# Optimization experiments

Measured on AMD Instinct MI355X. Metric: run time of the kernel, lower is better.

The kernel has to match this reference:

```python
import jax, jax.numpy as jnp
import numpy as np

EPS = 1e-6

def setup_inputs() -> dict:
    key = jax.random.key(0)
    ks = jax.random.split(key, 4)
    T, B, D, N = 512, 16, 1024, 512
    # xavier-uniform-ish scale for projections
    lim = float(np.sqrt(6.0 / (N + D)))
    x = jax.random.normal(ks[0], (T, B, D), dtype=jnp.float32)
    W_k = jax.random.uniform(ks[1], (N, D), minval=-lim, maxval=lim, dtype=jnp.float32)
    W_v = jax.random.uniform(ks[2], (N, D), minval=-lim, maxval=lim, dtype=jnp.float32)
    W_q = jax.random.uniform(ks[3], (N, D), minval=-lim, maxval=lim, dtype=jnp.float32)
    return {"x": x, "W_k": W_k, "W_v": W_v, "W_q": W_q}

def reference(x, W_k, W_v, W_q):
    # x: (T, B, D); delta-rule fast-weight cell, proj=no_z, nonlin=tanh,
    # gate=output, update=delta.
    T, B, D = x.shape
    n = W_k.shape[0]
    k = jnp.einsum('tbd,nd->tbn', x, W_k)
    v = jnp.einsum('tbd,nd->tbn', x, W_v)
    q = jnp.einsum('tbd,nd->tbn', x, W_q)
    k_norm = k / (jnp.linalg.norm(k, axis=-1, keepdims=True) + EPS)

    def step(S, kvq):
        k_t, v_t, q_t = kvq  # each (B, n)
        retrieved = jnp.einsum('bij,bj->bi', S, k_t)
        delta = v_t - retrieved
        S_new = jnp.tanh(S + delta[:, :, None] * k_t[:, None, :])
        Sq = jnp.einsum('bij,bj->bi', S_new, q_t)
        out = Sq * jax.nn.silu(Sq)
        return S_new, out

    S0 = jnp.zeros((B, n, n), dtype=x.dtype)
    S_final, outputs = jax.lax.scan(step, S0, (k_norm, v, q))
    return outputs, S_final
```

## Files before the change

kernel.cpp:

```cpp
#include <hip/hip_runtime.h>
#include <hip/hip_bf16.h>

#define T_DIM 512
#define B_DIM 16
#define D_DIM 1024
#define N_DIM 512

#define C_FOLD  2.885390082f
#define INV_C   0.3465735903f

typedef short s16x8 __attribute__((ext_vector_type(8)));
typedef float f32x4 __attribute__((ext_vector_type(4)));
typedef float f32x2 __attribute__((ext_vector_type(2)));

__device__ __forceinline__ unsigned short f2bf(float f) {
    unsigned u = __float_as_uint(f);
    unsigned r = (u + 0x7fffu + ((u >> 16) & 1u)) >> 16;
    return (unsigned short)r;
}

__device__ __forceinline__ float half32_sum(float x) {
    x += __int_as_float(__builtin_amdgcn_update_dpp(0, __float_as_int(x), 0xB1,  0xf, 0xf, true));
    x += __int_as_float(__builtin_amdgcn_update_dpp(0, __float_as_int(x), 0x4E,  0xf, 0xf, true));
    x += __int_as_float(__builtin_amdgcn_update_dpp(0, __float_as_int(x), 0x124, 0xf, 0xf, true));
    x += __int_as_float(__builtin_amdgcn_update_dpp(0, __float_as_int(x), 0x128, 0xf, 0xf, true));
    x += __int_as_float(__builtin_amdgcn_ds_swizzle(__float_as_int(x), 0x401F));
    return x;
}

__device__ __forceinline__ f32x2 tanh2p(f32x2 arg, f32x2 Cv, f32x2 M2Cv) {
    float e0 = __builtin_amdgcn_exp2f(arg.x) + 1.0f;
    float e1 = __builtin_amdgcn_exp2f(arg.y) + 1.0f;
    float r  = __builtin_amdgcn_rcpf(e0 * e1);
    f32x2 w; w.x = e1 * r; w.y = e0 * r;
    return Cv + w * M2Cv;
}

__global__ __launch_bounds__(256) void proj_gemm(
    const float* __restrict__ x,
    const float* __restrict__ Wk,
    const float* __restrict__ Wv,
    const float* __restrict__ Wq,
    float* __restrict__ kbuf, float* __restrict__ vbuf, float* __restrict__ qbuf)
{
    const float* W = (blockIdx.z == 0) ? Wk : (blockIdx.z == 1) ? Wv : Wq;
    float* out = (blockIdx.z == 0) ? kbuf : (blockIdx.z == 1) ? vbuf : qbuf;
    const float oscale = (blockIdx.z == 1) ? C_FOLD : 1.0f;

    __shared__ __align__(16) unsigned short As[64 * 40];
    __shared__ __align__(16) unsigned short Bs[64 * 40];

    const int tid  = threadIdx.x;
    const int m0   = blockIdx.x * 64;
    const int n0   = blockIdx.y * 64;
    const int wave = tid >> 6;
    const int lane = tid & 63;
    const int l15  = lane & 15;
    const int quad = lane >> 4;

    const int srow = tid >> 2;
    const int scol = (tid & 3) * 8;

    f32x4 acc[4];
#pragma unroll
    for (int i = 0; i < 4; ++i) acc[i] = (f32x4)0.0f;

    for (int k0 = 0; k0 < D_DIM; k0 += 32) {
        __syncthreads();
        {
            const float* srcA = &x[(size_t)(m0 + srow) * D_DIM + k0 + scol];
            float4 a0 = *(const float4*)srcA;
            float4 a1 = *(const float4*)(srcA + 4);
            uint4 pa;
            pa.x = (unsigned)f2bf(a0.x) | ((unsigned)f2bf(a0.y) << 16);
            pa.y = (unsigned)f2bf(a0.z) | ((unsigned)f2bf(a0.w) << 16);
            pa.z = (unsigned)f2bf(a1.x) | ((unsigned)f2bf(a1.y) << 16);
            pa.w = (unsigned)f2bf(a1.z) | ((unsigned)f2bf(a1.w) << 16);
            *(uint4*)&As[srow * 40 + scol] = pa;

            const float* srcB = &W[(size_t)(n0 + srow) * D_DIM + k0 + scol];
            float4 b0 = *(const float4*)srcB;
            float4 b1 = *(const float4*)(srcB + 4);
            uint4 pb;
            pb.x = (unsigned)f2bf(b0.x) | ((unsigned)f2bf(b0.y) << 16);
            pb.y = (unsigned)f2bf(b0.z) | ((unsigned)f2bf(b0.w) << 16);
            pb.z = (unsigned)f2bf(b1.x) | ((unsigned)f2bf(b1.y) << 16);
            pb.w = (unsigned)f2bf(b1.z) | ((unsigned)f2bf(b1.w) << 16);
            *(uint4*)&Bs[srow * 40 + scol] = pb;
        }
        __syncthreads();
        s16x8 af = *(const s16x8*)&As[(wave * 16 + l15) * 40 + quad * 8];
#pragma unroll
        for (int nt = 0; nt < 4; ++nt) {
            s16x8 bf = *(const s16x8*)&Bs[(nt * 16 + l15) * 40 + quad * 8];
            acc[nt] = __builtin_amdgcn_mfma_f32_16x16x32_bf16(af, bf, acc[nt], 0, 0, 0);
        }
    }
#pragma unroll
    for (int nt = 0; nt < 4; ++nt) {
#pragma unroll
        for (int rg = 0; rg < 4; ++rg) {
            int row = m0 + wave * 16 + quad * 4 + rg;
            int col = n0 + nt * 16 + l15;
            out[(size_t)row * N_DIM + col] = acc[nt][rg] * oscale;
        }
    }
}

__global__ __launch_bounds__(256) void knorm(float* __restrict__ kbuf)
{
    const int wave = threadIdx.x >> 6;
    const int lane = threadIdx.x & 63;
    const int row  = blockIdx.x * 4 + wave;
    float* p = &kbuf[(size_t)row * N_DIM + lane * 8];
    float4 a = *(const float4*)p;
    float4 b = *(const float4*)(p + 4);
    float s = a.x*a.x + a.y*a.y + a.z*a.z + a.w*a.w
            + b.x*b.x + b.y*b.y + b.z*b.z + b.w*b.w;
#pragma unroll
    for (int m = 1; m < 64; m <<= 1) s += __shfl_xor(s, m, 64);
    float inv = 1.0f / (sqrtf(s) + 1e-6f);
    a.x *= inv; a.y *= inv; a.z *= inv; a.w *= inv;
    b.x *= inv; b.y *= inv; b.z *= inv; b.w *= inv;
    *(float4*)p = a;
    *(float4*)(p + 4) = b;
}

__global__ __launch_bounds__(256) void scan_kernel(
    const float* __restrict__ kbuf, const float* __restrict__ vbuf,
    const float* __restrict__ qbuf, float* __restrict__ out)
{
    __shared__ __align__(16) float ks[2][528];
    __shared__ __align__(16) float qs[2][528];
    __shared__ float vs[2][16];

    const int tid  = threadIdx.x;
    const int lane = tid & 63;
    const int wv   = tid >> 6;
    const int h    = lane >> 5;
    const int tj   = lane & 31;
    const int b    = blockIdx.y;
    const int i0   = blockIdx.x * 16;
    const int r0   = 4 * wv + 2 * h;

    const int wA = 33 * (tid >> 4) + ((2 * tid) & 31);
    const int rA = 33 * (tj >> 1) + 16 * (tj & 1);

    f32x2 SA[8], SB[8];
#pragma unroll
    for (int u = 0; u < 8; ++u) { SA[u] = (f32x2)0.0f; SB[u] = (f32x2)0.0f; }

    float2 pk, pq; float pv = 0.0f;
    {
        const size_t o0 = (size_t)b * N_DIM;
        pk = *(const float2*)&kbuf[o0 + 2 * tid];
        pq = *(const float2*)&qbuf[o0 + 2 * tid];
        if (tid < 16) pv = vbuf[o0 + i0 + tid];
        *(float2*)&ks[0][wA] = pk;
        *(float2*)&qs[0][wA] = pq;
        if (tid < 16) vs[0][tid] = pv;
        const size_t o1 = (size_t)(B_DIM + b) * N_DIM;
        pk = *(const float2*)&kbuf[o1 + 2 * tid];
        pq = *(const float2*)&qbuf[o1 + 2 * tid];
        if (tid < 16) pv = vbuf[o1 + i0 + tid];
    }
    __syncthreads();

    const f32x2 Cv   = {C_FOLD, C_FOLD};
    const f32x2 M2Cv = {-2.0f * C_FOLD, -2.0f * C_FOLD};

    for (int t = 0; t < T_DIM; ++t) {
        const int cb = t & 1, nb = cb ^ 1;
        const size_t ofs = ((size_t)t * B_DIM + b) * N_DIM;

        if (t + 1 < T_DIM) {
            *(float2*)&ks[nb][wA] = pk;
            *(float2*)&qs[nb][wA] = pq;
            if (tid < 16) vs[nb][tid] = pv;
        }
        if (t + 2 < T_DIM) {
            const size_t o2 = ((size_t)(t + 2) * B_DIM + b) * N_DIM;
            pk = *(const float2*)&kbuf[o2 + 2 * tid];
            pq = *(const float2*)&qbuf[o2 + 2 * tid];
            if (tid < 16) pv = vbuf[o2 + i0 + tid];
        }

        f32x2 k2[8], q2[8];
#pragma unroll
        for (int u = 0; u < 4; ++u) {
            f32x4 kv = *(const f32x4*)&ks[cb][rA + 4 * u];
            f32x4 qv = *(const f32x4*)&qs[cb][rA + 4 * u];
            k2[2*u] = kv.xy; k2[2*u+1] = kv.zw;
            q2[2*u] = qv.xy; q2[2*u+1] = qv.zw;
        }
        const float v0 = vs[cb][r0];
        const float v1 = vs[cb][r0 + 1];

        f32x2 pa0 = (f32x2)0.0f, pb0 = (f32x2)0.0f;
        f32x2 pa1 = (f32x2)0.0f, pb1 = (f32x2)0.0f;
#pragma unroll
        for (int u = 0; u < 8; u += 2) {
            pa0 += SA[u] * k2[u];  pb0 += SA[u + 1] * k2[u + 1];
            pa1 += SB[u] * k2[u];  pb1 += SB[u + 1] * k2[u + 1];
        }
        const float racc0 = half32_sum(pa0.x + pa0.y + pb0.x + pb0.y);
        const float racc1 = half32_sum(pa1.x + pa1.y + pb1.x + pb1.y);

        const float dp0 = v0 - racc0;
        const float dp1 = v1 - racc1;
        const f32x2 d0 = {dp0, dp0}, d1 = {dp1, dp1};

        f32x2 sa0 = (f32x2)0.0f, sb0 = (f32x2)0.0f;
        f32x2 sa1 = (f32x2)0.0f, sb1 = (f32x2)0.0f;
#pragma unroll
        for (int u = 0; u < 8; u += 2) {
            f32x2 nA0 = tanh2p(SA[u]     + d0 * k2[u],     Cv, M2Cv);
            f32x2 nB0 = tanh2p(SB[u]     + d1 * k2[u],     Cv, M2Cv);
            f32x2 nA1 = tanh2p(SA[u + 1] + d0 * k2[u + 1], Cv, M2Cv);
            f32x2 nB1 = tanh2p(SB[u + 1] + d1 * k2[u + 1], Cv, M2Cv);
            SA[u] = nA0; SB[u] = nB0; SA[u + 1] = nA1; SB[u + 1] = nB1;
            sa0 += nA0 * q2[u];     sa1 += nB0 * q2[u];
            sb0 += nA1 * q2[u + 1]; sb1 += nB1 * q2[u + 1];
        }
        const float sq0 = half32_sum(sa0.x + sa0.y + sb0.x + sb0.y);
        const float sq1 = half32_sum(sa1.x + sa1.y + sb1.x + sb1.y);

        if (tj == 0) {
            float s0 = sq0 * INV_C, s1 = sq1 * INV_C;
            float g0 = __builtin_amdgcn_rcpf(1.0f + __builtin_amdgcn_exp2f(-s0 * 1.44269504f));
            float g1 = __builtin_amdgcn_rcpf(1.0f + __builtin_amdgcn_exp2f(-s1 * 1.44269504f));
            out[ofs + i0 + r0]     = s0 * s0 * g0;
            out[ofs + i0 + r0 + 1] = s1 * s1 * g1;
        }
        __syncthreads();
    }

    const size_t base = (size_t)T_DIM * B_DIM * N_DIM;
    const size_t so0 = base + ((size_t)b * N_DIM + i0 + r0) * N_DIM + 16 * tj;
    const size_t so1 = so0 + N_DIM;
#pragma unroll
    for (int u = 0; u < 4; ++u) {
        float4 w0, w1;
        w0.x = SA[2*u].x   * INV_C; w0.y = SA[2*u].y   * INV_C;
        w0.z = SA[2*u+1].x * INV_C; w0.w = SA[2*u+1].y * INV_C;
        w1.x = SB[2*u].x   * INV_C; w1.y = SB[2*u].y   * INV_C;
        w1.z = SB[2*u+1].x * INV_C; w1.w = SB[2*u+1].y * INV_C;
        *(float4*)&out[so0 + 4 * u] = w0;
        *(float4*)&out[so1 + 4 * u] = w1;
    }
}

extern "C" void kernel_launch(void* const* d_in, const int* in_sizes, int n_in,
                              void* d_out, int out_size, void* d_ws, size_t ws_size,
                              hipStream_t stream) {
    const float* x  = (const float*)d_in[0];
    const float* Wk = (const float*)d_in[1];
    const float* Wv = (const float*)d_in[2];
    const float* Wq = (const float*)d_in[3];
    float* outp = (float*)d_out;

    const size_t MN = (size_t)T_DIM * B_DIM * N_DIM;
    float* kbuf = (float*)d_ws;
    float* vbuf = kbuf + MN;
    float* qbuf = vbuf + MN;

    proj_gemm<<<dim3(128, 8, 3), 256, 0, stream>>>(x, Wk, Wv, Wq, kbuf, vbuf, qbuf);
    knorm<<<2048, 256, 0, stream>>>(kbuf);
    scan_kernel<<<dim3(32, 16), 256, 0, stream>>>(kbuf, vbuf, qbuf, outp);
}
```

Before: 797.1 us.

## Load k/q/v directly into registers per step, drop LDS staging and barriers

The scan loop no longer stages k, q and v through double-buffered shared memory with a block-wide barrier every timestep. Each lane now reads its own 16 k and 16 q values and its two v values straight from global memory into registers, one step ahead, with the loop unrolled by two to ping-pong between register sets. This removes the per-step __syncthreads and the LDS writes and reads. In exchange every lane issues redundant global loads (32 lanes share the same k/q slice, and each 16-row block rereads them), and the prefetch distance shrinks from two steps to one, so more global latency may be exposed.

```diff
diff --git a/kernel.cpp b/kernel.cpp
--- a/kernel.cpp
+++ b/kernel.cpp
@@ -130,10 +130,6 @@
     const float* __restrict__ kbuf, const float* __restrict__ vbuf,
     const float* __restrict__ qbuf, float* __restrict__ out)
 {
-    __shared__ __align__(16) float ks[2][528];
-    __shared__ __align__(16) float qs[2][528];
-    __shared__ float vs[2][16];
-
     const int tid  = threadIdx.x;
     const int lane = tid & 63;
     const int wv   = tid >> 6;
@@ -143,97 +139,90 @@
     const int i0   = blockIdx.x * 16;
     const int r0   = 4 * wv + 2 * h;
 
-    const int wA = 33 * (tid >> 4) + ((2 * tid) & 31);
-    const int rA = 33 * (tj >> 1) + 16 * (tj & 1);
+    const size_t BSTR = (size_t)B_DIM * N_DIM;
+    const float* kbase = kbuf + (size_t)b * N_DIM + 16 * tj;
+    const float* qbase = qbuf + (size_t)b * N_DIM + 16 * tj;
+    const float* vbase = vbuf + (size_t)b * N_DIM + i0 + r0;
 
     f32x2 SA[8], SB[8];
 #pragma unroll
     for (int u = 0; u < 8; ++u) { SA[u] = (f32x2)0.0f; SB[u] = (f32x2)0.0f; }
-
-    float2 pk, pq; float pv = 0.0f;
-    {
-        const size_t o0 = (size_t)b * N_DIM;
-        pk = *(const float2*)&kbuf[o0 + 2 * tid];
-        pq = *(const float2*)&qbuf[o0 + 2 * tid];
-        if (tid < 16) pv = vbuf[o0 + i0 + tid];
-        *(float2*)&ks[0][wA] = pk;
-        *(float2*)&qs[0][wA] = pq;
-        if (tid < 16) vs[0][tid] = pv;
-        const size_t o1 = (size_t)(B_DIM + b) * N_DIM;
-        pk = *(const float2*)&kbuf[o1 + 2 * tid];
-        pq = *(const float2*)&qbuf[o1 + 2 * tid];
-        if (tid < 16) pv = vbuf[o1 + i0 + tid];
-    }
-    __syncthreads();
 
     const f32x2 Cv   = {C_FOLD, C_FOLD};
     const f32x2 M2Cv = {-2.0f * C_FOLD, -2.0f * C_FOLD};
 
-    for (int t = 0; t < T_DIM; ++t) {
-        const int cb = t & 1, nb = cb ^ 1;
-        const size_t ofs = ((size_t)t * B_DIM + b) * N_DIM;
-
-        if (t + 1 < T_DIM) {
-            *(float2*)&ks[nb][wA] = pk;
-            *(float2*)&qs[nb][wA] = pq;
-            if (tid < 16) vs[nb][tid] = pv;
-        }
-        if (t + 2 < T_DIM) {
-            const size_t o2 = ((size_t)(t + 2) * B_DIM + b) * N_DIM;
-            pk = *(const float2*)&kbuf[o2 + 2 * tid];
-            pq = *(const float2*)&qbuf[o2 + 2 * tid];
-            if (tid < 16) pv = vbuf[o2 + i0 + tid];
-        }
-
-        f32x2 k2[8], q2[8];
-#pragma unroll
-        for (int u = 0; u < 4; ++u) {
-            f32x4 kv = *(const f32x4*)&ks[cb][rA + 4 * u];
-            f32x4 qv = *(const f32x4*)&qs[cb][rA + 4 * u];
-            k2[2*u] = kv.xy; k2[2*u+1] = kv.zw;
-            q2[2*u] = qv.xy; q2[2*u+1] = qv.zw;
-        }
-        const float v0 = vs[cb][r0];
-        const float v1 = vs[cb][r0 + 1];
-
-        f32x2 pa0 = (f32x2)0.0f, pb0 = (f32x2)0.0f;
-        f32x2 pa1 = (f32x2)0.0f, pb1 = (f32x2)0.0f;
-#pragma unroll
-        for (int u = 0; u < 8; u += 2) {
-            pa0 += SA[u] * k2[u];  pb0 += SA[u + 1] * k2[u + 1];
-            pa1 += SB[u] * k2[u];  pb1 += SB[u + 1] * k2[u + 1];
-        }
-        const float racc0 = half32_sum(pa0.x + pa0.y + pb0.x + pb0.y);
-        const float racc1 = half32_sum(pa1.x + pa1.y + pb1.x + pb1.y);
-
-        const float dp0 = v0 - racc0;
-        const float dp1 = v1 - racc1;
-        const f32x2 d0 = {dp0, dp0}, d1 = {dp1, dp1};
-
-        f32x2 sa0 = (f32x2)0.0f, sb0 = (f32x2)0.0f;
-        f32x2 sa1 = (f32x2)0.0f, sb1 = (f32x2)0.0f;
-#pragma unroll
-        for (int u = 0; u < 8; u += 2) {
-            f32x2 nA0 = tanh2p(SA[u]     + d0 * k2[u],     Cv, M2Cv);
-            f32x2 nB0 = tanh2p(SB[u]     + d1 * k2[u],     Cv, M2Cv);
-            f32x2 nA1 = tanh2p(SA[u + 1] + d0 * k2[u + 1], Cv, M2Cv);
-            f32x2 nB1 = tanh2p(SB[u + 1] + d1 * k2[u + 1], Cv, M2Cv);
-            SA[u] = nA0; SB[u] = nB0; SA[u + 1] = nA1; SB[u + 1] = nB1;
-            sa0 += nA0 * q2[u];     sa1 += nB0 * q2[u];
-            sb0 += nA1 * q2[u + 1]; sb1 += nB1 * q2[u + 1];
-        }
-        const float sq0 = half32_sum(sa0.x + sa0.y + sb0.x + sb0.y);
-        const float sq1 = half32_sum(sa1.x + sa1.y + sb1.x + sb1.y);
-
-        if (tj == 0) {
-            float s0 = sq0 * INV_C, s1 = sq1 * INV_C;
-            float g0 = __builtin_amdgcn_rcpf(1.0f + __builtin_amdgcn_exp2f(-s0 * 1.44269504f));
-            float g1 = __builtin_amdgcn_rcpf(1.0f + __builtin_amdgcn_exp2f(-s1 * 1.44269504f));
-            out[ofs + i0 + r0]     = s0 * s0 * g0;
-            out[ofs + i0 + r0 + 1] = s1 * s1 * g1;
-        }
-        __syncthreads();
-    }
+    f32x4 kA[4], qA[4], kB[4], qB[4];
+    float2 vA, vB;
+
+#pragma unroll
+    for (int u = 0; u < 4; ++u) {
+        kA[u] = *(const f32x4*)(kbase + 4 * u);
+        qA[u] = *(const f32x4*)(qbase + 4 * u);
+    }
+    vA = *(const float2*)vbase;
+
+#define SCAN_STEP(T_IDX, KC, QC, VC, KN, QN, VN)                              \
+    {                                                                         \
+        const int tn = ((T_IDX) + 1 < T_DIM) ? (T_IDX) + 1 : (T_DIM - 1);     \
+        const float* kpn = kbase + (size_t)tn * BSTR;                         \
+        const float* qpn = qbase + (size_t)tn * BSTR;                         \
+        _Pragma("unroll")                                                     \
+        for (int u = 0; u < 4; ++u) {                                         \
+            KN[u] = *(const f32x4*)(kpn + 4 * u);                             \
+            QN[u] = *(const f32x4*)(qpn + 4 * u);                             \
+        }                                                                     \
+        VN = *(const float2*)(vbase + (size_t)tn * BSTR);                     \
+                                                                              \
+        f32x2 k2[8], q2[8];                                                   \
+        _Pragma("unroll")                                                     \
+        for (int u = 0; u < 4; ++u) {                                         \
+            k2[2*u] = KC[u].xy; k2[2*u+1] = KC[u].zw;                         \
+            q2[2*u] = QC[u].xy; q2[2*u+1] = QC[u].zw;                         \
+        }                                                                     \
+                                                 \
+        f32x2 pa0 = (f32x2)0.0f, pb0 = (f32x2)0.0f;                           \
+        f32x2 pa1 = (f32x2)0.0f, pb1 = (f32x2)0.0f;                           \
+        _Pragma("unroll")                                                     \
+        for (int u = 0; u < 8; u += 2) {                                      \
+            pa0 += SA[u] * k2[u];  pb0 += SA[u + 1] * k2[u + 1];              \
+            pa1 += SB[u] * k2[u];  pb1 += SB[u + 1] * k2[u + 1];              \
+        }                                                                     \
+        const float racc0 = half32_sum(pa0.x + pa0.y + pb0.x + pb0.y);        \
+        const float racc1 = half32_sum(pa1.x + pa1.y + pb1.x + pb1.y);        \
+        const float dp0 = VC.x - racc0;                \
+        const float dp1 = VC.y - racc1;                                       \
+        const f32x2 d0 = {dp0, dp0}, d1 = {dp1, dp1};                         \
+        f32x2 sa0 = (f32x2)0.0f, sb0 = (f32x2)0.0f;                           \
+        f32x2 sa1 = (f32x2)0.0f, sb1 = (f32x2)0.0f;                           \
+        _Pragma("unroll")                                                     \
+        for (int u = 0; u < 8; u += 2) {                                      \
+            f32x2 nA0 = tanh2p(SA[u]     + d0 * k2[u],     Cv, M2Cv);         \
+            f32x2 nB0 = tanh2p(SB[u]     + d1 * k2[u],     Cv, M2Cv);         \
+            f32x2 nA1 = tanh2p(SA[u + 1] + d0 * k2[u + 1], Cv, M2Cv);         \
+            f32x2 nB1 = tanh2p(SB[u + 1] + d1 * k2[u + 1], Cv, M2Cv);         \
+            SA[u] = nA0; SB[u] = nB0; SA[u + 1] = nA1; SB[u + 1] = nB1;       \
+            sa0 += nA0 * q2[u];     sa1 += nB0 * q2[u];                       \
+            sb0 += nA1 * q2[u + 1]; sb1 += nB1 * q2[u + 1];                   \
+        }                                                                     \
+        const float sq0 = half32_sum(sa0.x + sa0.y + sb0.x + sb0.y);          \
+        const float sq1 = half32_sum(sa1.x + sa1.y + sb1.x + sb1.y);          \
+        if (tj == 0) {                                                        \
+            const size_t ofs = (size_t)(T_IDX) * BSTR + (size_t)b * N_DIM;    \
+            float s0 = sq0 * INV_C, s1 = sq1 * INV_C;                         \
+            float g0 = __builtin_amdgcn_rcpf(                                 \
+                1.0f + __builtin_amdgcn_exp2f(-s0 * 1.44269504f));            \
+            float g1 = __builtin_amdgcn_rcpf(                                 \
+                1.0f + __builtin_amdgcn_exp2f(-s1 * 1.44269504f));            \
+            out[ofs + i0 + r0]     = s0 * s0 * g0;                            \
+            out[ofs + i0 + r0 + 1] = s1 * s1 * g1;                            \
+        }                                                                     \
+    }
+
+    for (int t = 0; t < T_DIM; t += 2) {
+        SCAN_STEP(t,     kA, qA, vA, kB, qB, vB)
+        SCAN_STEP(t + 1, kB, qB, vB, kA, qA, vA)
+    }
+#undef SCAN_STEP
 
     const size_t base = (size_t)T_DIM * B_DIM * N_DIM;
     const size_t so0 = base + ((size_t)b * N_DIM + i0 + r0) * N_DIM + 16 * tj;
```

Result: slower. 827.2 us (+3.8%).
